# Optimization experiments

Measured on AMD Instinct MI355X. Metric: run time of the kernel, lower is better.

The kernel has to match this reference:

```python
import jax, jax.numpy as jnp
import numpy as np

DIMS = [1, 3, 5]  # irrep dims 2l+1 for l=0,1,2 (maxdim=3)
PAIRS = {0: [(0,0),(1,1),(2,2)],
         1: [(0,1),(1,0),(1,1),(1,2),(2,1)],
         2: [(0,2),(1,1),(1,2),(2,0),(2,1),(2,2)]}
B, N, C = 8, 128, 32

def setup_inputs() -> dict:
    key = jax.random.key(0)
    ks = iter(jax.random.split(key, 64))
    inp = {}
    for l, d in enumerate(DIMS):
        inp[f"atom_{l}"] = jax.random.normal(next(ks), (B, N, C, d), jnp.float32)
        inp[f"edge_{l}"] = jax.random.normal(next(ks), (B, N, N, C, d), jnp.float32)
    inp["mask"] = jax.random.randint(next(ks), (B, N, N), 0, 2).astype(bool)
    for l, prs in PAIRS.items():
        for (l1, l2) in prs:
            d1, d2, d = DIMS[l1], DIMS[l2], DIMS[l]
            inp[f"cg_{l1}{l2}{l}"] = jax.random.normal(next(ks), (d1, d2, d), jnp.float32) / np.float32((d1 * d2) ** 0.5)
    for l in range(3):
        cin = (2 * len(PAIRS[l]) + 1) * C  # [aggregate pairs | identity | self-power pairs] * C
        gain = np.float32(2.0 / cin ** 0.5)  # level_gain=2.0, randn init
        inp[f"w_{l}"] = jax.random.normal(next(ks), (cin, C), jnp.float32) * gain
    return inp

def reference(atom_0, atom_1, atom_2, edge_0, edge_1, edge_2, mask,
              cg_000, cg_110, cg_220, cg_011, cg_101, cg_111, cg_121, cg_211,
              cg_022, cg_112, cg_122, cg_202, cg_212, cg_222, w_0, w_1, w_2):
    atoms = [atom_0, atom_1, atom_2]
    edges = [edge_0, edge_1, edge_2]
    cg = {(0,0,0): cg_000, (1,1,0): cg_110, (2,2,0): cg_220,
          (0,1,1): cg_011, (1,0,1): cg_101, (1,1,1): cg_111, (1,2,1): cg_121, (2,1,1): cg_211,
          (0,2,2): cg_022, (1,1,2): cg_112, (1,2,2): cg_122, (2,0,2): cg_202, (2,1,2): cg_212, (2,2,2): cg_222}
    ws = [w_0, w_1, w_2]
    m = mask.astype(atom_0.dtype)  # [B,N,N] edge mask
    outs = []
    for l in range(3):
        parts = []
        # cg_aggregate: neighbor-summed CG tensor product atom[j] x edge[i,j]
        for (l1, l2) in PAIRS[l]:
            parts.append(jnp.einsum('bjcx,bijcy,bij,xyz->bicz',
                                    atoms[l1], edges[l2], m, cg[(l1, l2, l)]))
        # identity (pass-through of atom reps)
        parts.append(atoms[l])
        # cg_power: self CG tensor product atom[i] x atom[i]
        for (l1, l2) in PAIRS[l]:
            parts.append(jnp.einsum('bicx,bicy,xyz->bicz',
                                    atoms[l1], atoms[l2], cg[(l1, l2, l)]))
        cat = jnp.concatenate(parts, axis=2)  # [B,N,Ctot_l,d_l]
        outs.append(jnp.einsum('bnkz,ko->bnoz', cat, ws[l]))  # channel mix -> [B,N,C,d_l]
    return tuple(outs)
```

## Files before the change

### kernel.cpp

```cpp
#include <hip/hip_runtime.h>

#define BB 8
#define NN 128
#define CC 32

struct Params {
  const float* __restrict__ atom0; const float* __restrict__ atom1; const float* __restrict__ atom2;
  const float* __restrict__ edge0; const float* __restrict__ edge1; const float* __restrict__ edge2;
  const void*  mask;
  const float* __restrict__ cg[14];
  const float* __restrict__ w0; const float* __restrict__ w1; const float* __restrict__ w2;
  float* __restrict__ out;
};

__global__ __launch_bounds__(512, 2) void lgn_fused(Params p) {
  const int tid = threadIdx.x;
  const int c   = tid & 31;
  const int s   = tid >> 5;
  const int sx  = s >> 3;
  const int jp  = s & 7;
  const int blk = blockIdx.x;
  const int b   = blk & 7;
  const int i   = blk >> 3;

  __shared__ float arena[9216];
  __shared__ float sm_cg[540];
  __shared__ float sm_ai[288];
  __shared__ int   sm_list[128];
  __shared__ int   sm_nact, sm_mode;

  if (tid == 0) sm_mode = 0;
  __syncthreads();
  if (tid < 64) {
    unsigned v = ((const unsigned*)p.mask)[tid];
    if (v == 0x3F800000u) atomicOr(&sm_mode, 2);
    else if (v > 1u)      atomicOr(&sm_mode, 1);
  }
  {
    constexpr int CGSZ[14] = {1,9,25, 9,9,27,45,45, 25,45,75,25,75,125};
    constexpr int CGOF[14] = {0,1,10, 35,44,53,80,125, 170,195,240,315,340,415};
    #pragma unroll
    for (int t = 0; t < 14; ++t)
      for (int idx = tid; idx < CGSZ[t]; idx += 512)
        sm_cg[CGOF[t] + idx] = p.cg[t][idx];
    const int nodeBase = (b * NN + i) * CC;
    for (int s2 = tid; s2 < 288; s2 += 512) {
      int cc = s2 / 9, comp = s2 - cc * 9;
      float v;
      if (comp == 0)      v = p.atom0[nodeBase + cc];
      else if (comp < 4)  v = p.atom1[(nodeBase + cc) * 3 + comp - 1];
      else                v = p.atom2[(nodeBase + cc) * 5 + comp - 4];
      sm_ai[s2] = v;
    }
  }
  __syncthreads();
  const int mode = (sm_mode & 2) ? 2 : sm_mode;

  if (tid < 64) {
    const int row = (b * NN + i) * NN;
    bool mv0, mv1;
    if (mode == 0) {
      mv0 = ((const int*)p.mask)[row + tid] != 0;
      mv1 = ((const int*)p.mask)[row + tid + 64] != 0;
    } else if (mode == 2) {
      mv0 = ((const float*)p.mask)[row + tid] != 0.f;
      mv1 = ((const float*)p.mask)[row + tid + 64] != 0.f;
    } else {
      mv0 = ((const unsigned char*)p.mask)[row + tid] != 0;
      mv1 = ((const unsigned char*)p.mask)[row + tid + 64] != 0;
    }
    unsigned long long b0 = __ballot(mv0);
    unsigned long long b1 = __ballot(mv1);
    int n0 = (int)__popcll(b0);
    unsigned long long lt = (1ull << tid) - 1ull;
    if (mv0) sm_list[__popcll(b0 & lt)] = tid;
    if (mv1) sm_list[n0 + __popcll(b1 & lt)] = tid + 64;
    if (tid == 0) sm_nact = n0 + (int)__popcll(b1);
  }
  __syncthreads();
  const int nact = sm_nact;
  const int nt   = (nact + 7) >> 3;
  if (tid < 64) {
    const int j0 = (nact > 0) ? sm_list[0] : 0;
    if (tid      >= nact && tid      < 128) sm_list[tid]      = j0;
    if (tid + 64 >= nact && tid + 64 < 128) sm_list[tid + 64] = j0;
  }
  __syncthreads();

  const float* srcB[3]; int jmul[3], dstO[3], jgk[3];
  {
    const long ab = (long)b * NN;
    const long eb = (long)(b * NN + i) * NN;
    #pragma unroll
    for (int k = 0; k < 3; ++k) {
      const int f  = tid + k * 512;
      const int jg = f / 144;
      const int r  = f - jg * 144;
      jgk[k] = jg;
      if (r < 8)        { srcB[k] = p.atom0 + ab *  32 + r * 4;        jmul[k] =  32; dstO[k] = jg * 576 +   0 + r * 4; }
      else if (r < 32)  { int q = r - 8;   srcB[k] = p.atom1 + ab *  96 + q * 4; jmul[k] =  96; dstO[k] = jg * 576 +  32 + q * 4; }
      else if (r < 72)  { int q = r - 32;  srcB[k] = p.atom2 + ab * 160 + q * 4; jmul[k] = 160; dstO[k] = jg * 576 + 128 + q * 4; }
      else if (r < 80)  { int q = r - 72;  srcB[k] = p.edge0 + eb *  32 + q * 4; jmul[k] =  32; dstO[k] = jg * 576 + 288 + q * 4; }
      else if (r < 104) { int q = r - 80;  srcB[k] = p.edge1 + eb *  96 + q * 4; jmul[k] =  96; dstO[k] = jg * 576 + 320 + q * 4; }
      else              { int q = r - 104; srcB[k] = p.edge2 + eb * 160 + q * 4; jmul[k] = 160; dstO[k] = jg * 576 + 416 + q * 4; }
    }
  }

  float acc[5][9];
  #pragma unroll
  for (int k = 0; k < 5; ++k)
    #pragma unroll
    for (int y = 0; y < 9; ++y) acc[k][y] = 0.f;

  if (nt > 0) {
    float4 v0, v1, v2;
    v0 = *(const float4*)(srcB[0] + (long)sm_list[jgk[0]] * jmul[0]);
    v1 = *(const float4*)(srcB[1] + (long)sm_list[jgk[1]] * jmul[1]);
    if (tid < 128) v2 = *(const float4*)(srcB[2] + (long)sm_list[jgk[2]] * jmul[2]);
    *(float4*)(arena + dstO[0]) = v0;
    *(float4*)(arena + dstO[1]) = v1;
    if (tid < 128) *(float4*)(arena + dstO[2]) = v2;
    __syncthreads();

    for (int t = 0; t < nt; ++t) {
      const bool more = (t + 1 < nt);
      if (more) {
        const int base = (t + 1) * 8;
        v0 = *(const float4*)(srcB[0] + (long)sm_list[base + jgk[0]] * jmul[0]);
        v1 = *(const float4*)(srcB[1] + (long)sm_list[base + jgk[1]] * jmul[1]);
        if (tid < 128) v2 = *(const float4*)(srcB[2] + (long)sm_list[base + jgk[2]] * jmul[2]);
      }
      {
        const float* bp = arena + (t & 1) * 4608 + jp * 576;
        const float wt = (t * 8 + jp < nact) ? 1.f : 0.f;
        float e[9];
        e[0] = bp[288 + c];
        #pragma unroll
        for (int y = 0; y < 3; ++y) e[1 + y] = bp[320 + c * 3 + y];
        #pragma unroll
        for (int y = 0; y < 5; ++y) e[4 + y] = bp[416 + c * 5 + y];
        if (sx == 0) {
          float a[4];
          a[0] = bp[c];
          #pragma unroll
          for (int y = 0; y < 3; ++y) a[1 + y] = bp[32 + c * 3 + y];
          #pragma unroll
          for (int k = 0; k < 4; ++k) {
            const float av = a[k] * wt;
            #pragma unroll
            for (int y = 0; y < 9; ++y) acc[k][y] += av * e[y];
          }
        } else {
          float a[5];
          #pragma unroll
          for (int y = 0; y < 5; ++y) a[y] = bp[128 + c * 5 + y];
          #pragma unroll
          for (int k = 0; k < 5; ++k) {
            const float av = a[k] * wt;
            #pragma unroll
            for (int y = 0; y < 9; ++y) acc[k][y] += av * e[y];
          }
        }
      }
      if (more) {
        float* bp = arena + ((t + 1) & 1) * 4608;
        *(float4*)(bp + dstO[0]) = v0;
        *(float4*)(bp + dstO[1]) = v1;
        if (tid < 128) *(float4*)(bp + dstO[2]) = v2;
      }
      __syncthreads();
    }
  }

  const int sc = sx * 32 + c;
  if (jp >= 6) {
    float* sp = &arena[(jp - 6) * 2880 + sc];
    #pragma unroll
    for (int k = 0; k < 5; ++k)
      #pragma unroll
      for (int y = 0; y < 9; ++y) sp[(k * 9 + y) * 64] = acc[k][y];
  }
  __syncthreads();
  if (jp == 4 || jp == 5) {
    const float* sp = &arena[(jp - 4) * 2880 + sc];
    #pragma unroll
    for (int k = 0; k < 5; ++k)
      #pragma unroll
      for (int y = 0; y < 9; ++y) acc[k][y] += sp[(k * 9 + y) * 64];
  }
  __syncthreads();
  if (jp == 4 || jp == 5) {
    float* sp = &arena[(jp - 4) * 2880 + sc];
    #pragma unroll
    for (int k = 0; k < 5; ++k)
      #pragma unroll
      for (int y = 0; y < 9; ++y) sp[(k * 9 + y) * 64] = acc[k][y];
  }
  __syncthreads();
  if (jp <= 1) {
    const float* sp = &arena[jp * 2880 + sc];
    #pragma unroll
    for (int k = 0; k < 5; ++k)
      #pragma unroll
      for (int y = 0; y < 9; ++y) acc[k][y] += sp[(k * 9 + y) * 64];
  }
  __syncthreads();
  if (jp == 2 || jp == 3) {
    float* sp = &arena[(jp - 2) * 2880 + sc];
    #pragma unroll
    for (int k = 0; k < 5; ++k)
      #pragma unroll
      for (int y = 0; y < 9; ++y) sp[(k * 9 + y) * 64] = acc[k][y];
  }
  __syncthreads();
  if (jp <= 1) {
    const float* sp = &arena[jp * 2880 + sc];
    #pragma unroll
    for (int k = 0; k < 5; ++k)
      #pragma unroll
      for (int y = 0; y < 9; ++y) acc[k][y] += sp[(k * 9 + y) * 64];
  }
  #pragma unroll
  for (int k = 0; k < 5; ++k)
    #pragma unroll
    for (int y = 0; y < 9; ++y) acc[k][y] += __shfl_down(acc[k][y], 32);
  __syncthreads();

  if (s == 0) {
    #pragma unroll
    for (int k = 0; k < 4; ++k)
      #pragma unroll
      for (int y = 0; y < 9; ++y) arena[c * 81 + k * 9 + y] = acc[k][y];
  } else if (s == 8) {
    #pragma unroll
    for (int k = 0; k < 5; ++k)
      #pragma unroll
      for (int y = 0; y < 9; ++y) arena[c * 81 + (4 + k) * 9 + y] = acc[k][y];
  }
  __syncthreads();

  {
    constexpr int colL[31]   = {0,0,0,0,0,0,0, 1,1,1,1,1,1,1,1,1,1,1, 2,2,2,2,2,2,2,2,2,2,2,2,2};
    constexpr int colKind[31]= {0,0,0,1,2,2,2, 0,0,0,0,0,1,2,2,2,2,2, 0,0,0,0,0,0,1,2,2,2,2,2,2};
    constexpr int colL1[31]  = {0,1,2,0,0,1,2, 0,1,1,1,2,0,0,1,1,1,2, 0,1,1,2,2,2,0,0,1,1,2,2,2};
    constexpr int colL2[31]  = {0,1,2,0,0,1,2, 1,0,1,2,1,0,1,0,1,2,1, 2,1,2,0,1,2,0,2,1,2,0,1,2};
    constexpr int colCg[31]  = {0,1,10,0,0,1,10, 35,44,53,80,125,0,35,44,53,80,125,
                                170,195,240,315,340,415,0,170,195,240,315,340,415};
    constexpr int colP[31]   = {0,1,2,3,4,5,6, 0,1,2,3,4,5,6,7,8,9,10, 0,1,2,3,4,5,6,7,8,9,10,11,12};
    constexpr int DD[3]      = {1,3,5};
    constexpr int catBase[3] = {0,224,1280};
    constexpr int aOff[3]    = {0,1,4};

    for (int col = s; col < 31; col += 16) {
      const int l = colL[col];
      const int d = DD[l];
      const int kind = colKind[col];
      float* catp = &arena[2592 + catBase[l] + (colP[col] * CC + c) * d];
      if (kind == 1) {
        for (int z = 0; z < d; ++z) catp[z] = sm_ai[c * 9 + aOff[l] + z];
      } else if (kind == 0) {
        const int l1 = colL1[col], l2 = colL2[col];
        const int d1 = DD[l1], d2 = DD[l2];
        const int x0 = aOff[l1], y0 = aOff[l2];
        const float* cgp = &sm_cg[colCg[col]];
        const float* Ofl = &arena[c * 81];
        for (int z = 0; z < d; ++z) {
          float sum = 0.f;
          for (int xi = 0; xi < d1; ++xi)
            for (int yi = 0; yi < d2; ++yi)
              sum += Ofl[(x0 + xi) * 9 + y0 + yi] * cgp[(xi * d2 + yi) * d + z];
          catp[z] = sum;
        }
      } else {
        const int l1 = colL1[col], l2 = colL2[col];
        const int d1 = DD[l1], d2 = DD[l2];
        const float* cgp = &sm_cg[colCg[col]];
        const float* a1p = &sm_ai[c * 9 + aOff[l1]];
        const float* a2p = &sm_ai[c * 9 + aOff[l2]];
        for (int z = 0; z < d; ++z) {
          float sum = 0.f;
          for (int xi = 0; xi < d1; ++xi)
            for (int yi = 0; yi < d2; ++yi)
              sum += a1p[xi] * a2p[yi] * cgp[(xi * d2 + yi) * d + z];
          catp[z] = sum;
        }
      }
    }
  }
  __syncthreads();

  {
    float accm[9];
    #pragma unroll
    for (int q = 0; q < 9; ++q) accm[q] = 0.f;
    const int co = c;
    #pragma unroll
    for (int k0 = 0; k0 < 224; k0 += 16) {
      const int k = k0 + s;
      accm[0] += arena[2592 + k] * p.w0[k * CC + co];
    }
    #pragma unroll
    for (int k0 = 0; k0 < 352; k0 += 16) {
      const int k = k0 + s;
      float wv = p.w1[k * CC + co];
      accm[1] += arena[2592 + 224 + k * 3 + 0] * wv;
      accm[2] += arena[2592 + 224 + k * 3 + 1] * wv;
      accm[3] += arena[2592 + 224 + k * 3 + 2] * wv;
    }
    #pragma unroll
    for (int k0 = 0; k0 < 416; k0 += 16) {
      const int k = k0 + s;
      float wv = p.w2[k * CC + co];
      #pragma unroll
      for (int z = 0; z < 5; ++z)
        accm[4 + z] += arena[2592 + 1280 + k * 5 + z] * wv;
    }
    #pragma unroll
    for (int q = 0; q < 9; ++q) accm[q] += __shfl_down(accm[q], 32);
    if ((s & 1) == 0) {
      #pragma unroll
      for (int q = 0; q < 9; ++q)
        arena[5952 + (s >> 1) * 288 + co * 9 + q] = accm[q];
    }
  }
  __syncthreads();

  if (tid < 288) {
    float v = 0.f;
    #pragma unroll
    for (int gg = 0; gg < 8; ++gg) v += arena[5952 + gg * 288 + tid];
    const int co = tid / 9, zz = tid - co * 9;
    const int nb = (b * NN + i) * CC;
    int oidx;
    if (zz == 0)     oidx = nb + co;
    else if (zz < 4) oidx = 32768  + (nb + co) * 3 + (zz - 1);
    else             oidx = 131072 + (nb + co) * 5 + (zz - 4);
    p.out[oidx] = v;
  }
}

extern "C" void kernel_launch(void* const* d_in, const int* in_sizes, int n_in,
                              void* d_out, int out_size, void* d_ws, size_t ws_size,
                              hipStream_t stream) {
  Params p;
  const bool interleaved = (in_sizes[1] == BB * NN * NN * CC);
  if (interleaved) {
    p.atom0 = (const float*)d_in[0]; p.edge0 = (const float*)d_in[1];
    p.atom1 = (const float*)d_in[2]; p.edge1 = (const float*)d_in[3];
    p.atom2 = (const float*)d_in[4]; p.edge2 = (const float*)d_in[5];
  } else {
    p.atom0 = (const float*)d_in[0]; p.atom1 = (const float*)d_in[1]; p.atom2 = (const float*)d_in[2];
    p.edge0 = (const float*)d_in[3]; p.edge1 = (const float*)d_in[4]; p.edge2 = (const float*)d_in[5];
  }
  p.mask = d_in[6];
  for (int t = 0; t < 14; ++t) p.cg[t] = (const float*)d_in[7 + t];
  p.w0 = (const float*)d_in[21];
  p.w1 = (const float*)d_in[22];
  p.w2 = (const float*)d_in[23];
  p.out = (float*)d_out;

  lgn_fused<<<dim3(BB * NN), dim3(512), 0, stream>>>(p);
}
```

Before: 67.62 us.

## Split fused kernel into dense aggregation and channel-mix kernels via workspace

Splits the single fused kernel into two launches. The aggregation kernel now streams all 128 neighbours densely with a fixed 16-step, two-stage unrolled prefetch, weighting each neighbour by a mask value held in shared memory, instead of compacting the active neighbours into a list. It writes the CG-aggregated features to a global workspace. A second kernel builds the concatenated features and does the channel mix, with the weight columns preloaded into registers. This removes the serialized tail of the fused kernel and the ballot-based compaction, but it reads masked-out neighbours' data, adds a launch and a workspace round trip, and needs heavy register use in the mix kernel.

Result: slower. 126.3 us (+86.8%).

```diff
diff --git a/kernel.cpp b/kernel.cpp
--- a/kernel.cpp
+++ b/kernel.cpp
@@ -4,16 +4,23 @@
 #define NN 128
 #define CC 32
 
-struct Params {
+struct ParamsA {
   const float* __restrict__ atom0; const float* __restrict__ atom1; const float* __restrict__ atom2;
   const float* __restrict__ edge0; const float* __restrict__ edge1; const float* __restrict__ edge2;
   const void*  mask;
   const float* __restrict__ cg[14];
+  float* __restrict__ ws;
+};
+
+struct ParamsB {
+  const float* __restrict__ atom0; const float* __restrict__ atom1; const float* __restrict__ atom2;
+  const float* __restrict__ cg[14];
   const float* __restrict__ w0; const float* __restrict__ w1; const float* __restrict__ w2;
+  const float* __restrict__ ws;
   float* __restrict__ out;
 };
 
-__global__ __launch_bounds__(512, 2) void lgn_fused(Params p) {
+__global__ __launch_bounds__(512, 2) void lgn_agg(ParamsA p) {
   const int tid = threadIdx.x;
   const int c   = tid & 31;
   const int s   = tid >> 5;
@@ -25,9 +32,8 @@
 
   __shared__ float arena[9216];
   __shared__ float sm_cg[540];
-  __shared__ float sm_ai[288];
-  __shared__ int   sm_list[128];
-  __shared__ int   sm_nact, sm_mode;
+  __shared__ float sm_wts[128];
+  __shared__ int   sm_mode;
 
   if (tid == 0) sm_mode = 0;
   __syncthreads();
@@ -43,8 +49,230 @@
     for (int t = 0; t < 14; ++t)
       for (int idx = tid; idx < CGSZ[t]; idx += 512)
         sm_cg[CGOF[t] + idx] = p.cg[t][idx];
-    const int nodeBase = (b * NN + i) * CC;
-    for (int s2 = tid; s2 < 288; s2 += 512) {
+  }
+  __syncthreads();
+  const int mode = (sm_mode & 2) ? 2 : sm_mode;
+
+  if (tid < 128) {
+    const int midx = (b * NN + i) * NN + tid;
+    bool mv;
+    if (mode == 0)      mv = ((const int*)p.mask)[midx] != 0;
+    else if (mode == 2) mv = ((const float*)p.mask)[midx] != 0.f;
+    else                mv = ((const unsigned char*)p.mask)[midx] != 0;
+    sm_wts[tid] = mv ? 1.f : 0.f;
+  }
+
+  const float* srcB[3]; int jmul[3], dstO[3], jgk[3];
+  {
+    const long ab = (long)b * NN;
+    const long eb = (long)(b * NN + i) * NN;
+    #pragma unroll
+    for (int k = 0; k < 3; ++k) {
+      const int f  = tid + k * 512;
+      const int jg = f / 144;
+      const int r  = f - jg * 144;
+      jgk[k] = jg;
+      if (r < 8)        { srcB[k] = p.atom0 + ab *  32 + r * 4;              jmul[k] =  32; dstO[k] = jg * 576 +   0 + r * 4; }
+      else if (r < 32)  { int q = r - 8;   srcB[k] = p.atom1 + ab *  96 + q * 4; jmul[k] =  96; dstO[k] = jg * 576 +  32 + q * 4; }
+      else if (r < 72)  { int q = r - 32;  srcB[k] = p.atom2 + ab * 160 + q * 4; jmul[k] = 160; dstO[k] = jg * 576 + 128 + q * 4; }
+      else if (r < 80)  { int q = r - 72;  srcB[k] = p.edge0 + eb *  32 + q * 4; jmul[k] =  32; dstO[k] = jg * 576 + 288 + q * 4; }
+      else if (r < 104) { int q = r - 80;  srcB[k] = p.edge1 + eb *  96 + q * 4; jmul[k] =  96; dstO[k] = jg * 576 + 320 + q * 4; }
+      else              { int q = r - 104; srcB[k] = p.edge2 + eb * 160 + q * 4; jmul[k] = 160; dstO[k] = jg * 576 + 416 + q * 4; }
+    }
+  }
+
+  float acc[5][9];
+  #pragma unroll
+  for (int k = 0; k < 5; ++k)
+    #pragma unroll
+    for (int y = 0; y < 9; ++y) acc[k][y] = 0.f;
+
+#define LOADG(V0, V1, V2, G) do {                                           \
+    V0 = *(const float4*)(srcB[0] + (long)((G) * 8 + jgk[0]) * jmul[0]);    \
+    V1 = *(const float4*)(srcB[1] + (long)((G) * 8 + jgk[1]) * jmul[1]);    \
+    if (tid < 128)                                                          \
+      V2 = *(const float4*)(srcB[2] + (long)((G) * 8 + jgk[2]) * jmul[2]);  \
+  } while (0)
+
+#define WRITEG(V0, V1, V2, G) do {                                          \
+    float* bp_ = arena + ((G) & 1) * 4608;                                  \
+    *(float4*)(bp_ + dstO[0]) = V0;                                         \
+    *(float4*)(bp_ + dstO[1]) = V1;                                         \
+    if (tid < 128) *(float4*)(bp_ + dstO[2]) = V2;                          \
+  } while (0)
+
+#define CONSUME(T) do {                                                     \
+    const float* bp = arena + ((T) & 1) * 4608 + jp * 576;                  \
+    const float wt = sm_wts[(T) * 8 + jp];                                  \
+    float e[9];                                                             \
+    e[0] = bp[288 + c];                                                     \
+    _Pragma("unroll")                                                       \
+    for (int y = 0; y < 3; ++y) e[1 + y] = bp[320 + c * 3 + y];             \
+    _Pragma("unroll")                                                       \
+    for (int y = 0; y < 5; ++y) e[4 + y] = bp[416 + c * 5 + y];             \
+    if (sx == 0) {                                                          \
+      float a[4];                                                           \
+      a[0] = bp[c];                                                         \
+      _Pragma("unroll")                                                     \
+      for (int y = 0; y < 3; ++y) a[1 + y] = bp[32 + c * 3 + y];            \
+      _Pragma("unroll")                                                     \
+      for (int k = 0; k < 4; ++k) {                                         \
+        const float av = a[k] * wt;                                         \
+        _Pragma("unroll")                                                   \
+        for (int y = 0; y < 9; ++y) acc[k][y] += av * e[y];                 \
+      }                                                                     \
+    } else {                                                                \
+      float a[5];                                                           \
+      _Pragma("unroll")                                                     \
+      for (int y = 0; y < 5; ++y) a[y] = bp[128 + c * 5 + y];               \
+      _Pragma("unroll")                                                     \
+      for (int k = 0; k < 5; ++k) {                                         \
+        const float av = a[k] * wt;                                         \
+        _Pragma("unroll")                                                   \
+        for (int y = 0; y < 9; ++y) acc[k][y] += av * e[y];                 \
+      }                                                                     \
+    }                                                                       \
+  } while (0)
+
+  {
+    float4 c0, c1, c2, n0, n1, n2;
+    LOADG(c0, c1, c2, 0);
+    WRITEG(c0, c1, c2, 0);
+    LOADG(c0, c1, c2, 1);
+    __syncthreads();
+    for (int T = 0; T < 16; T += 2) {
+      if (T + 2 < 16) LOADG(n0, n1, n2, T + 2);
+      CONSUME(T);
+      WRITEG(c0, c1, c2, T + 1);
+      __syncthreads();
+      if (T + 3 < 16) LOADG(c0, c1, c2, T + 3);
+      CONSUME(T + 1);
+      if (T + 2 < 16) WRITEG(n0, n1, n2, T + 2);
+      __syncthreads();
+    }
+  }
+#undef LOADG
+#undef WRITEG
+#undef CONSUME
+
+  const int sc = sx * 32 + c;
+  if (jp >= 6) {
+    float* sp = &arena[(jp - 6) * 2880 + sc];
+    #pragma unroll
+    for (int k = 0; k < 5; ++k)
+      #pragma unroll
+      for (int y = 0; y < 9; ++y) sp[(k * 9 + y) * 64] = acc[k][y];
+  }
+  __syncthreads();
+  if (jp == 4 || jp == 5) {
+    const float* sp = &arena[(jp - 4) * 2880 + sc];
+    #pragma unroll
+    for (int k = 0; k < 5; ++k)
+      #pragma unroll
+      for (int y = 0; y < 9; ++y) acc[k][y] += sp[(k * 9 + y) * 64];
+  }
+  __syncthreads();
+  if (jp == 4 || jp == 5) {
+    float* sp = &arena[(jp - 4) * 2880 + sc];
+    #pragma unroll
+    for (int k = 0; k < 5; ++k)
+      #pragma unroll
+      for (int y = 0; y < 9; ++y) sp[(k * 9 + y) * 64] = acc[k][y];
+  }
+  __syncthreads();
+  if (jp <= 1) {
+    const float* sp = &arena[jp * 2880 + sc];
+    #pragma unroll
+    for (int k = 0; k < 5; ++k)
+      #pragma unroll
+      for (int y = 0; y < 9; ++y) acc[k][y] += sp[(k * 9 + y) * 64];
+  }
+  __syncthreads();
+  if (jp == 2 || jp == 3) {
+    float* sp = &arena[(jp - 2) * 2880 + sc];
+    #pragma unroll
+    for (int k = 0; k < 5; ++k)
+      #pragma unroll
+      for (int y = 0; y < 9; ++y) sp[(k * 9 + y) * 64] = acc[k][y];
+  }
+  __syncthreads();
+  if (jp <= 1) {
+    const float* sp = &arena[jp * 2880 + sc];
+    #pragma unroll
+    for (int k = 0; k < 5; ++k)
+      #pragma unroll
+      for (int y = 0; y < 9; ++y) acc[k][y] += sp[(k * 9 + y) * 64];
+  }
+  #pragma unroll
+  for (int k = 0; k < 5; ++k)
+    #pragma unroll
+    for (int y = 0; y < 9; ++y) acc[k][y] += __shfl_down(acc[k][y], 32);
+  __syncthreads();
+
+  if (s == 0) {
+    #pragma unroll
+    for (int k = 0; k < 4; ++k)
+      #pragma unroll
+      for (int y = 0; y < 9; ++y) arena[c * 81 + k * 9 + y] = acc[k][y];
+  } else if (s == 8) {
+    #pragma unroll
+    for (int k = 0; k < 5; ++k)
+      #pragma unroll
+      for (int y = 0; y < 9; ++y) arena[c * 81 + (4 + k) * 9 + y] = acc[k][y];
+  }
+  __syncthreads();
+
+  {
+    constexpr int aggD[14]  = {1,1,1, 3,3,3,3,3, 5,5,5,5,5,5};
+    constexpr int aggL1[14] = {0,1,2, 0,1,1,1,2, 0,1,1,2,2,2};
+    constexpr int aggL2[14] = {0,1,2, 1,0,1,2,1, 2,1,2,0,1,2};
+    constexpr int aggCg[14] = {0,1,10, 35,44,53,80,125, 170,195,240,315,340,415};
+    constexpr int aggF[14]  = {0,1,2, 3,6,9,12,15, 18,23,28,33,38,43};
+    constexpr int DD[3]     = {1,3,5};
+    constexpr int aOff[3]   = {0,1,4};
+    const long wsbase = (long)(b * NN + i) * 1536;
+    if (s < 14) {
+      const int col = s;
+      const int d = aggD[col], f0 = aggF[col];
+      const int l1 = aggL1[col], l2 = aggL2[col];
+      const int d1 = DD[l1], d2 = DD[l2];
+      const int x0 = aOff[l1], y0 = aOff[l2];
+      const float* cgp = &sm_cg[aggCg[col]];
+      const float* Ofl = &arena[c * 81];
+      for (int z = 0; z < d; ++z) {
+        float sum = 0.f;
+        for (int xi = 0; xi < d1; ++xi)
+          for (int yi = 0; yi < d2; ++yi)
+            sum += Ofl[(x0 + xi) * 9 + y0 + yi] * cgp[(xi * d2 + yi) * d + z];
+        p.ws[wsbase + (f0 + z) * 32 + c] = sum;
+      }
+    }
+  }
+}
+
+__global__ __launch_bounds__(256, 1) void lgn_mix(ParamsB p) {
+  const int tid = threadIdx.x;
+  const int c   = tid & 31;
+  const int g   = tid >> 5;
+  const int blk = blockIdx.x;
+  const int b   = blk & 7;
+  const int i   = blk >> 3;
+  const int node = b * NN + i;
+
+  __shared__ float sm_cat[3360];
+  __shared__ float sm_cg[540];
+  __shared__ float sm_ai[288];
+  __shared__ float sm_mix[1152];
+
+  {
+    constexpr int CGSZ[14] = {1,9,25, 9,9,27,45,45, 25,45,75,25,75,125};
+    constexpr int CGOF[14] = {0,1,10, 35,44,53,80,125, 170,195,240,315,340,415};
+    #pragma unroll
+    for (int t = 0; t < 14; ++t)
+      for (int idx = tid; idx < CGSZ[t]; idx += 256)
+        sm_cg[CGOF[t] + idx] = p.cg[t][idx];
+    const int nodeBase = node * CC;
+    for (int s2 = tid; s2 < 288; s2 += 256) {
       int cc = s2 / 9, comp = s2 - cc * 9;
       float v;
       if (comp == 0)      v = p.atom0[nodeBase + cc];
@@ -54,190 +282,8 @@
     }
   }
   __syncthreads();
-  const int mode = (sm_mode & 2) ? 2 : sm_mode;
-
-  if (tid < 64) {
-    const int row = (b * NN + i) * NN;
-    bool mv0, mv1;
-    if (mode == 0) {
-      mv0 = ((const int*)p.mask)[row + tid] != 0;
-      mv1 = ((const int*)p.mask)[row + tid + 64] != 0;
-    } else if (mode == 2) {
-      mv0 = ((const float*)p.mask)[row + tid] != 0.f;
-      mv1 = ((const float*)p.mask)[row + tid + 64] != 0.f;
-    } else {
-      mv0 = ((const unsigned char*)p.mask)[row + tid] != 0;
-      mv1 = ((const unsigned char*)p.mask)[row + tid + 64] != 0;
-    }
-    unsigned long long b0 = __ballot(mv0);
-    unsigned long long b1 = __ballot(mv1);
-    int n0 = (int)__popcll(b0);
-    unsigned long long lt = (1ull << tid) - 1ull;
-    if (mv0) sm_list[__popcll(b0 & lt)] = tid;
-    if (mv1) sm_list[n0 + __popcll(b1 & lt)] = tid + 64;
-    if (tid == 0) sm_nact = n0 + (int)__popcll(b1);
-  }
-  __syncthreads();
-  const int nact = sm_nact;
-  const int nt   = (nact + 7) >> 3;
-  if (tid < 64) {
-    const int j0 = (nact > 0) ? sm_list[0] : 0;
-    if (tid      >= nact && tid      < 128) sm_list[tid]      = j0;
-    if (tid + 64 >= nact && tid + 64 < 128) sm_list[tid + 64] = j0;
-  }
-  __syncthreads();
-
-  const float* srcB[3]; int jmul[3], dstO[3], jgk[3];
-  {
-    const long ab = (long)b * NN;
-    const long eb = (long)(b * NN + i) * NN;
-    #pragma unroll
-    for (int k = 0; k < 3; ++k) {
-      const int f  = tid + k * 512;
-      const int jg = f / 144;
-      const int r  = f - jg * 144;
-      jgk[k] = jg;
-      if (r < 8)        { srcB[k] = p.atom0 + ab *  32 + r * 4;        jmul[k] =  32; dstO[k] = jg * 576 +   0 + r * 4; }
-      else if (r < 32)  { int q = r - 8;   srcB[k] = p.atom1 + ab *  96 + q * 4; jmul[k] =  96; dstO[k] = jg * 576 +  32 + q * 4; }
-      else if (r < 72)  { int q = r - 32;  srcB[k] = p.atom2 + ab * 160 + q * 4; jmul[k] = 160; dstO[k] = jg * 576 + 128 + q * 4; }
-      else if (r < 80)  { int q = r - 72;  srcB[k] = p.edge0 + eb *  32 + q * 4; jmul[k] =  32; dstO[k] = jg * 576 + 288 + q * 4; }
-      else if (r < 104) { int q = r - 80;  srcB[k] = p.edge1 + eb *  96 + q * 4; jmul[k] =  96; dstO[k] = jg * 576 + 320 + q * 4; }
-      else              { int q = r - 104; srcB[k] = p.edge2 + eb * 160 + q * 4; jmul[k] = 160; dstO[k] = jg * 576 + 416 + q * 4; }
-    }
-  }
-
-  float acc[5][9];
-  #pragma unroll
-  for (int k = 0; k < 5; ++k)
-    #pragma unroll
-    for (int y = 0; y < 9; ++y) acc[k][y] = 0.f;
-
-  if (nt > 0) {
-    float4 v0, v1, v2;
-    v0 = *(const float4*)(srcB[0] + (long)sm_list[jgk[0]] * jmul[0]);
-    v1 = *(const float4*)(srcB[1] + (long)sm_list[jgk[1]] * jmul[1]);
-    if (tid < 128) v2 = *(const float4*)(srcB[2] + (long)sm_list[jgk[2]] * jmul[2]);
-    *(float4*)(arena + dstO[0]) = v0;
-    *(float4*)(arena + dstO[1]) = v1;
-    if (tid < 128) *(float4*)(arena + dstO[2]) = v2;
-    __syncthreads();
-
-    for (int t = 0; t < nt; ++t) {
-      const bool more = (t + 1 < nt);
-      if (more) {
-        const int base = (t + 1) * 8;
-        v0 = *(const float4*)(srcB[0] + (long)sm_list[base + jgk[0]] * jmul[0]);
-        v1 = *(const float4*)(srcB[1] + (long)sm_list[base + jgk[1]] * jmul[1]);
-        if (tid < 128) v2 = *(const float4*)(srcB[2] + (long)sm_list[base + jgk[2]] * jmul[2]);
-      }
-      {
-        const float* bp = arena + (t & 1) * 4608 + jp * 576;
-        const float wt = (t * 8 + jp < nact) ? 1.f : 0.f;
-        float e[9];
-        e[0] = bp[288 + c];
-        #pragma unroll
-        for (int y = 0; y < 3; ++y) e[1 + y] = bp[320 + c * 3 + y];
-        #pragma unroll
-        for (int y = 0; y < 5; ++y) e[4 + y] = bp[416 + c * 5 + y];
-        if (sx == 0) {
-          float a[4];
-          a[0] = bp[c];
-          #pragma unroll
-          for (int y = 0; y < 3; ++y) a[1 + y] = bp[32 + c * 3 + y];
-          #pragma unroll
-          for (int k = 0; k < 4; ++k) {
-            const float av = a[k] * wt;
-            #pragma unroll
-            for (int y = 0; y < 9; ++y) acc[k][y] += av * e[y];
-          }
-        } else {
-          float a[5];
-          #pragma unroll
-          for (int y = 0; y < 5; ++y) a[y] = bp[128 + c * 5 + y];
-          #pragma unroll
-          for (int k = 0; k < 5; ++k) {
-            const float av = a[k] * wt;
-            #pragma unroll
-            for (int y = 0; y < 9; ++y) acc[k][y] += av * e[y];
-          }
-        }
-      }
-      if (more) {
-        float* bp = arena + ((t + 1) & 1) * 4608;
-        *(float4*)(bp + dstO[0]) = v0;
-        *(float4*)(bp + dstO[1]) = v1;
-        if (tid < 128) *(float4*)(bp + dstO[2]) = v2;
-      }
-      __syncthreads();
-    }
-  }
-
-  const int sc = sx * 32 + c;
-  if (jp >= 6) {
-    float* sp = &arena[(jp - 6) * 2880 + sc];
-    #pragma unroll
-    for (int k = 0; k < 5; ++k)
-      #pragma unroll
-      for (int y = 0; y < 9; ++y) sp[(k * 9 + y) * 64] = acc[k][y];
-  }
-  __syncthreads();
-  if (jp == 4 || jp == 5) {
-    const float* sp = &arena[(jp - 4) * 2880 + sc];
-    #pragma unroll
-    for (int k = 0; k < 5; ++k)
-      #pragma unroll
-      for (int y = 0; y < 9; ++y) acc[k][y] += sp[(k * 9 + y) * 64];
-  }
-  __syncthreads();
-  if (jp == 4 || jp == 5) {
-    float* sp = &arena[(jp - 4) * 2880 + sc];
-    #pragma unroll
-    for (int k = 0; k < 5; ++k)
-      #pragma unroll
-      for (int y = 0; y < 9; ++y) sp[(k * 9 + y) * 64] = acc[k][y];
-  }
-  __syncthreads();
-  if (jp <= 1) {
-    const float* sp = &arena[jp * 2880 + sc];
-    #pragma unroll
-    for (int k = 0; k < 5; ++k)
-      #pragma unroll
-      for (int y = 0; y < 9; ++y) acc[k][y] += sp[(k * 9 + y) * 64];
-  }
-  __syncthreads();
-  if (jp == 2 || jp == 3) {
-    float* sp = &arena[(jp - 2) * 2880 + sc];
-    #pragma unroll
-    for (int k = 0; k < 5; ++k)
-      #pragma unroll
-      for (int y = 0; y < 9; ++y) sp[(k * 9 + y) * 64] = acc[k][y];
-  }
-  __syncthreads();
-  if (jp <= 1) {
-    const float* sp = &arena[jp * 2880 + sc];
-    #pragma unroll
-    for (int k = 0; k < 5; ++k)
-      #pragma unroll
-      for (int y = 0; y < 9; ++y) acc[k][y] += sp[(k * 9 + y) * 64];
-  }
-  #pragma unroll
-  for (int k = 0; k < 5; ++k)
-    #pragma unroll
-    for (int y = 0; y < 9; ++y) acc[k][y] += __shfl_down(acc[k][y], 32);
-  __syncthreads();
-
-  if (s == 0) {
-    #pragma unroll
-    for (int k = 0; k < 4; ++k)
-      #pragma unroll
-      for (int y = 0; y < 9; ++y) arena[c * 81 + k * 9 + y] = acc[k][y];
-  } else if (s == 8) {
-    #pragma unroll
-    for (int k = 0; k < 5; ++k)
-      #pragma unroll
-      for (int y = 0; y < 9; ++y) arena[c * 81 + (4 + k) * 9 + y] = acc[k][y];
-  }
-  __syncthreads();
+
+  const float* wsp = p.ws + (long)node * 1536;
 
   {
     constexpr int colL[31]   = {0,0,0,0,0,0,0, 1,1,1,1,1,1,1,1,1,1,1, 2,2,2,2,2,2,2,2,2,2,2,2,2};
@@ -247,30 +293,22 @@
     constexpr int colCg[31]  = {0,1,10,0,0,1,10, 35,44,53,80,125,0,35,44,53,80,125,
                                 170,195,240,315,340,415,0,170,195,240,315,340,415};
     constexpr int colP[31]   = {0,1,2,3,4,5,6, 0,1,2,3,4,5,6,7,8,9,10, 0,1,2,3,4,5,6,7,8,9,10,11,12};
+    constexpr int colF[31]   = {0,1,2,-1,-1,-1,-1, 3,6,9,12,15,-1,-1,-1,-1,-1,-1,
+                                18,23,28,33,38,43,-1,-1,-1,-1,-1,-1,-1};
     constexpr int DD[3]      = {1,3,5};
     constexpr int catBase[3] = {0,224,1280};
     constexpr int aOff[3]    = {0,1,4};
 
-    for (int col = s; col < 31; col += 16) {
+    for (int col = g; col < 31; col += 8) {
       const int l = colL[col];
       const int d = DD[l];
       const int kind = colKind[col];
-      float* catp = &arena[2592 + catBase[l] + (colP[col] * CC + c) * d];
-      if (kind == 1) {
+      float* catp = &sm_cat[catBase[l] + (colP[col] * CC + c) * d];
+      if (kind == 0) {
+        const int f0 = colF[col];
+        for (int z = 0; z < d; ++z) catp[z] = wsp[(f0 + z) * 32 + c];
+      } else if (kind == 1) {
         for (int z = 0; z < d; ++z) catp[z] = sm_ai[c * 9 + aOff[l] + z];
-      } else if (kind == 0) {
-        const int l1 = colL1[col], l2 = colL2[col];
-        const int d1 = DD[l1], d2 = DD[l2];
-        const int x0 = aOff[l1], y0 = aOff[l2];
-        const float* cgp = &sm_cg[colCg[col]];
-        const float* Ofl = &arena[c * 81];
-        for (int z = 0; z < d; ++z) {
-          float sum = 0.f;
-          for (int xi = 0; xi < d1; ++xi)
-            for (int yi = 0; yi < d2; ++yi)
-              sum += Ofl[(x0 + xi) * 9 + y0 + yi] * cgp[(xi * d2 + yi) * d + z];
-          catp[z] = sum;
-        }
       } else {
         const int l1 = colL1[col], l2 = colL2[col];
         const int d1 = DD[l1], d2 = DD[l2];
@@ -287,50 +325,53 @@
       }
     }
   }
+
+  float w0r[28], w1r[44], w2r[52];
+  #pragma unroll
+  for (int u = 0; u < 28; ++u) w0r[u] = p.w0[(g + u * 8) * CC + c];
+  #pragma unroll
+  for (int u = 0; u < 44; ++u) w1r[u] = p.w1[(g + u * 8) * CC + c];
+  #pragma unroll
+  for (int u = 0; u < 52; ++u) w2r[u] = p.w2[(g + u * 8) * CC + c];
   __syncthreads();
 
   {
     float accm[9];
     #pragma unroll
     for (int q = 0; q < 9; ++q) accm[q] = 0.f;
-    const int co = c;
-    #pragma unroll
-    for (int k0 = 0; k0 < 224; k0 += 16) {
-      const int k = k0 + s;
-      accm[0] += arena[2592 + k] * p.w0[k * CC + co];
-    }
-    #pragma unroll
-    for (int k0 = 0; k0 < 352; k0 += 16) {
-      const int k = k0 + s;
-      float wv = p.w1[k * CC + co];
-      accm[1] += arena[2592 + 224 + k * 3 + 0] * wv;
-      accm[2] += arena[2592 + 224 + k * 3 + 1] * wv;
-      accm[3] += arena[2592 + 224 + k * 3 + 2] * wv;
-    }
-    #pragma unroll
-    for (int k0 = 0; k0 < 416; k0 += 16) {
-      const int k = k0 + s;
-      float wv = p.w2[k * CC + co];
+    #pragma unroll
+    for (int u = 0; u < 28; ++u)
+      accm[0] += sm_cat[g + u * 8] * w0r[u];
+    #pragma unroll
+    for (int u = 0; u < 44; ++u) {
+      const int k = g + u * 8;
+      const float wv = w1r[u];
+      accm[1] += sm_cat[224 + k * 3 + 0] * wv;
+      accm[2] += sm_cat[224 + k * 3 + 1] * wv;
+      accm[3] += sm_cat[224 + k * 3 + 2] * wv;
+    }
+    #pragma unroll
+    for (int u = 0; u < 52; ++u) {
+      const int k = g + u * 8;
+      const float wv = w2r[u];
       #pragma unroll
       for (int z = 0; z < 5; ++z)
-        accm[4 + z] += arena[2592 + 1280 + k * 5 + z] * wv;
+        accm[4 + z] += sm_cat[1280 + k * 5 + z] * wv;
     }
     #pragma unroll
     for (int q = 0; q < 9; ++q) accm[q] += __shfl_down(accm[q], 32);
-    if ((s & 1) == 0) {
+    if ((g & 1) == 0) {
       #pragma unroll
       for (int q = 0; q < 9; ++q)
-        arena[5952 + (s >> 1) * 288 + co * 9 + q] = accm[q];
-    }
-  }
-  __syncthreads();
-
-  if (tid < 288) {
-    float v = 0.f;
-    #pragma unroll
-    for (int gg = 0; gg < 8; ++gg) v += arena[5952 + gg * 288 + tid];
-    const int co = tid / 9, zz = tid - co * 9;
-    const int nb = (b * NN + i) * CC;
+        sm_mix[(g >> 1) * 288 + c * 9 + q] = accm[q];
+    }
+  }
+  __syncthreads();
+
+  for (int s2 = tid; s2 < 288; s2 += 256) {
+    float v = sm_mix[s2] + sm_mix[288 + s2] + sm_mix[576 + s2] + sm_mix[864 + s2];
+    const int co = s2 / 9, zz = s2 - co * 9;
+    const int nb = node * CC;
     int oidx;
     if (zz == 0)     oidx = nb + co;
     else if (zz < 4) oidx = 32768  + (nb + co) * 3 + (zz - 1);
@@ -342,22 +383,33 @@
 extern "C" void kernel_launch(void* const* d_in, const int* in_sizes, int n_in,
                               void* d_out, int out_size, void* d_ws, size_t ws_size,
                               hipStream_t stream) {
-  Params p;
+  const float *atom0, *atom1, *atom2, *edge0, *edge1, *edge2;
   const bool interleaved = (in_sizes[1] == BB * NN * NN * CC);
   if (interleaved) {
-    p.atom0 = (const float*)d_in[0]; p.edge0 = (const float*)d_in[1];
-    p.atom1 = (const float*)d_in[2]; p.edge1 = (const float*)d_in[3];
-    p.atom2 = (const float*)d_in[4]; p.edge2 = (const float*)d_in[5];
+    atom0 = (const float*)d_in[0]; edge0 = (const float*)d_in[1];
+    atom1 = (const float*)d_in[2]; edge1 = (const float*)d_in[3];
+    atom2 = (const float*)d_in[4]; edge2 = (const float*)d_in[5];
   } else {
-    p.atom0 = (const float*)d_in[0]; p.atom1 = (const float*)d_in[1]; p.atom2 = (const float*)d_in[2];
-    p.edge0 = (const float*)d_in[3]; p.edge1 = (const float*)d_in[4]; p.edge2 = (const float*)d_in[5];
-  }
-  p.mask = d_in[6];
-  for (int t = 0; t < 14; ++t) p.cg[t] = (const float*)d_in[7 + t];
-  p.w0 = (const float*)d_in[21];
-  p.w1 = (const float*)d_in[22];
-  p.w2 = (const float*)d_in[23];
-  p.out = (float*)d_out;
-
-  lgn_fused<<<dim3(BB * NN), dim3(512), 0, stream>>>(p);
+    atom0 = (const float*)d_in[0]; atom1 = (const float*)d_in[1]; atom2 = (const float*)d_in[2];
+    edge0 = (const float*)d_in[3]; edge1 = (const float*)d_in[4]; edge2 = (const float*)d_in[5];
+  }
+
+  ParamsA pa;
+  pa.atom0 = atom0; pa.atom1 = atom1; pa.atom2 = atom2;
+  pa.edge0 = edge0; pa.edge1 = edge1; pa.edge2 = edge2;
+  pa.mask  = d_in[6];
+  for (int t = 0; t < 14; ++t) pa.cg[t] = (const float*)d_in[7 + t];
+  pa.ws = (float*)d_ws;
+
+  ParamsB pb;
+  pb.atom0 = atom0; pb.atom1 = atom1; pb.atom2 = atom2;
+  for (int t = 0; t < 14; ++t) pb.cg[t] = (const float*)d_in[7 + t];
+  pb.w0 = (const float*)d_in[21];
+  pb.w1 = (const float*)d_in[22];
+  pb.w2 = (const float*)d_in[23];
+  pb.ws = (const float*)d_ws;
+  pb.out = (float*)d_out;
+
+  lgn_agg<<<dim3(BB * NN), dim3(512), 0, stream>>>(pa);
+  lgn_mix<<<dim3(BB * NN), dim3(256), 0, stream>>>(pb);
 }
```
